# Kernel tuning notes

Measured on AMD Instinct MI355X. Metric: run time of the kernel, lower is better.

The kernel has to match this reference:

```python
import jax, jax.numpy as jnp
import numpy as np

K, T, CIN = 30000, 35, 7
EPS = 1e-5  # torch BatchNorm default


def _bn(x, gamma, beta):
    # x: [1, K, T, C]; per-channel batch-stat normalization over (0,1,2)
    mean = jnp.mean(x, axis=(0, 1, 2))
    var = jnp.var(x, axis=(0, 1, 2))
    return (x - mean) * jax.lax.rsqrt(var + EPS) * gamma + beta


def _vfe(x, mask, W, b, gamma, beta):
    # x: [1, K, T, Cin] -> [1, K, T, 2*units]
    pw = jnp.einsum('bkti,iu->bktu', x, W) + b
    pw = jax.nn.relu(_bn(pw, gamma, beta))
    agg = jnp.max(pw, axis=2, keepdims=True)            # [1, K, 1, units]
    out = jnp.concatenate([pw, jnp.broadcast_to(agg, pw.shape)], axis=-1)
    return out * mask


def setup_inputs() -> dict:
    key = jax.random.key(0)
    ks = jax.random.split(key, 8)
    inp = {}
    inp['x'] = jax.random.normal(ks[0], (K, T, CIN), jnp.float32)
    inp['coordinate'] = jax.random.randint(ks[1], (K, 4), 0, 1, dtype=jnp.int32)
    inp['batch_size'] = 1
    inp['W1'] = jax.random.normal(ks[2], (7, 16), jnp.float32) * 0.3
    inp['b1'] = jnp.zeros((16,), jnp.float32)
    inp['g1'] = jnp.ones((16,), jnp.float32)
    inp['be1'] = jnp.zeros((16,), jnp.float32)
    inp['W2'] = jax.random.normal(ks[3], (32, 64), jnp.float32) * 0.15
    inp['b2'] = jnp.zeros((64,), jnp.float32)
    inp['g2'] = jnp.ones((64,), jnp.float32)
    inp['be2'] = jnp.zeros((64,), jnp.float32)
    inp['Wd'] = jax.random.normal(ks[4], (128, 128), jnp.float32) * 0.1
    inp['bd'] = jnp.zeros((128,), jnp.float32)
    inp['gd'] = jnp.ones((128,), jnp.float32)
    inp['bed'] = jnp.zeros((128,), jnp.float32)
    return inp


def reference(x, coordinate, batch_size, W1, b1, g1, be1, W2, b2, g2, be2, Wd, bd, gd, bed):
    xb = x[None]                                   # [1, K, T, 7]
    # mask: 1 where the point's feature sum is nonzero
    mask = (jnp.sum(xb, axis=-1) != 0.0).astype(jnp.float32)[..., None]  # [1,K,T,1]
    h = _vfe(xb, mask, W1, b1, g1, be1)            # [1, K, T, 32]
    h = _vfe(h, mask, W2, b2, g2, be2)             # [1, K, T, 128]
    h = jnp.einsum('bktc,cd->bktd', h, Wd) + bd    # [1, K, T, 128]
    h = _bn(h, gd, bed)                            # BatchNorm2d after permute(0,3,1,2)
    h = jnp.where(h >= 0, h, 0.1 * h)              # leaky_relu(0.1)
    h = jnp.max(h, axis=2)                         # max over points -> [1, K, 128]
    out = jnp.transpose(h, (0, 2, 1))              # [1, 128, K] to match NCHW layout
    return (out, coordinate)
```

## Files before the change

kernel.cpp:

```cpp
#include <hip/hip_runtime.h>

#define KVOX 30000
#define TP 35
#define NPTS (KVOX * TP)
#define EPS_BN 1e-5f

typedef __attribute__((ext_vector_type(8))) short short8_t;
typedef __attribute__((ext_vector_type(4))) float f32x4;

#define SLOTG_OFF 0
#define SLOT2_OFF 2560
#define SLOT3_OFF 10752
#define PAR_A1 27136
#define PAR_C1 27152
#define PAR_A2 27168
#define PAR_C2 27232
#define PAR_A3 27296
#define PAR_C3 27424
#define STATS_FLOATS 27136
#define W2T_OFF 27552
#define WDT_OFF 28576
#define M3_OFF 36768
#define SMALL_FLOATS (36768 + KVOX * 128)
#define H1G_OFF SMALL_FLOATS
#define AGG1G_OFF (H1G_OFF + KVOX * 280)
#define MASKG_OFF (AGG1G_OFF + KVOX * 8)
#define FULL_FLOATS (MASKG_OFF + (KVOX * 35 + 1) / 2)

__device__ __forceinline__ ushort f2bf(float f) {
    uint r;
    asm("v_cvt_pk_bf16_f32 %0, %1, %2" : "=v"(r) : "v"(f), "v"(f));
    return (ushort)r;
}
__device__ __forceinline__ uint f2bf2(float lo, float hi) {
    uint r;
    asm("v_cvt_pk_bf16_f32 %0, %1, %2" : "=v"(r) : "v"(lo), "v"(hi));
    return r;
}
__device__ __forceinline__ float bf2f(ushort h) {
    union { uint u; float f; } v; v.u = ((uint)h) << 16; return v.f;
}

__global__ __launch_bounds__(256) void k_prep_stats1(
    const float* __restrict__ x,
    const float* __restrict__ W2, const float* __restrict__ Wd,
    const float* __restrict__ gd,
    ushort* __restrict__ w2t, ushort* __restrict__ wdt,
    float* __restrict__ slotG) {
    if (blockIdx.x < 64) {
        int t = blockIdx.x * 256 + threadIdx.x;
        if (t < 2048) {
            int u = t >> 5, k = t & 31;
            w2t[t] = f2bf(W2[k * 64 + u]);
        }
        int u = t >> 7, k = t & 127;
        float sg = (gd[u] < 0.f) ? -1.f : 1.f;
        wdt[t] = f2bf(Wd[k * 128 + u] * sg);
        return;
    }
    int bid = blockIdx.x - 64;
    int tid = threadIdx.x;
    int gid = bid * 256 + tid;
    float sx[7], G[28];
#pragma unroll
    for (int c = 0; c < 7; ++c) sx[c] = 0.f;
#pragma unroll
    for (int i = 0; i < 28; ++i) G[i] = 0.f;
    for (int p = gid; p < NPTS; p += 256 * 256) {
        const float* xp = x + (size_t)p * 7;
        float xv[7];
#pragma unroll
        for (int c = 0; c < 7; ++c) { xv[c] = xp[c]; sx[c] += xv[c]; }
        int idx = 0;
#pragma unroll
        for (int i = 0; i < 7; ++i)
#pragma unroll
            for (int j = i; j < 7; ++j) { G[idx] = fmaf(xv[i], xv[j], G[idx]); ++idx; }
    }
    int lane = tid & 63;
    int wv = tid >> 6;
    int slot = (bid * 4 + wv) & 63;
#pragma unroll
    for (int k = 0; k < 35; ++k) {
        float v = (k < 28) ? G[k] : sx[k - 28];
#pragma unroll
        for (int m = 32; m > 0; m >>= 1) v += __shfl_xor(v, m, 64);
        if (lane == 0) atomicAdd(&slotG[slot * 40 + k], v);
    }
}

__global__ void k_affine1g(const float* __restrict__ slotG,
                           const float* __restrict__ W1, const float* __restrict__ b1,
                           const float* __restrict__ g1, const float* __restrict__ be1,
                           float* __restrict__ pa, float* __restrict__ pc, float invN) {
    __shared__ float red[35];
    int t = threadIdx.x;
    if (t < 35) {
        float s = 0.f;
#pragma unroll
        for (int sl = 0; sl < 64; ++sl) s += slotG[sl * 40 + t];
        red[t] = s;
    }
    __syncthreads();
    if (t < 16) {
        float wv[7];
#pragma unroll
        for (int c = 0; c < 7; ++c) wv[c] = W1[c * 16 + t];
        float b = b1[t];
        float sw = 0.f;
#pragma unroll
        for (int c = 0; c < 7; ++c) sw = fmaf(red[28 + c], wv[c], sw);
        float gq = 0.f;
        int idx = 0;
#pragma unroll
        for (int i = 0; i < 7; ++i)
#pragma unroll
            for (int j = i; j < 7; ++j) {
                float coef = wv[i] * wv[j];
                if (i != j) coef *= 2.f;
                gq = fmaf(coef, red[idx], gq);
                ++idx;
            }
        float mr = sw * invN;
        float mean = mr + b;
        float ex2 = gq * invN + 2.f * b * mr + b * b;
        float var = ex2 - mean * mean;
        float av = g1[t] * rsqrtf(var + EPS_BN);
        pa[t] = av;
        pc[t] = be1[t] - mean * av;
    }
}

__global__ void k_affine_b(const float* __restrict__ slots,
                           const float* __restrict__ g,
                           const float* __restrict__ be,
                           const float* __restrict__ bias,
                           float* __restrict__ pa, float* __restrict__ pc,
                           int C, float invN) {
    int u = threadIdx.x;
    if (u >= C) return;
    float s = 0.f, q = 0.f;
    for (int sl = 0; sl < 64; ++sl) {
        s += slots[sl * 2 * C + u];
        q += slots[sl * 2 * C + C + u];
    }
    float b = bias[u];
    float mr = s * invN;
    float mean = mr + b;
    float ex2 = q * invN + 2.f * b * mr + b * b;
    float var = ex2 - mean * mean;
    float av = g[u] * rsqrtf(var + EPS_BN);
    pa[u] = av;
    pc[u] = be[u] - mean * av;
}

__global__ void k_affine_b3(const float* __restrict__ slots,
                            const float* __restrict__ g,
                            const float* __restrict__ be,
                            const float* __restrict__ bias,
                            float* __restrict__ pa, float* __restrict__ pc,
                            int C, float invN) {
    int u = threadIdx.x;
    if (u >= C) return;
    float s = 0.f, q = 0.f;
    for (int sl = 0; sl < 64; ++sl) {
        s += slots[sl * 2 * C + u];
        q += slots[sl * 2 * C + C + u];
    }
    float sg = (g[u] < 0.f) ? -1.f : 1.f;
    s *= sg;
    float b = bias[u];
    float mr = s * invN;
    float mean = mr + b;
    float ex2 = q * invN + 2.f * b * mr + b * b;
    float var = ex2 - mean * mean;
    float av = g[u] * rsqrtf(var + EPS_BN);
    pa[u] = av;
    pc[u] = be[u] - mean * av;
}

__device__ __forceinline__ void phaseA(
    int k0, int tid,
    const float* __restrict__ x,
    const float* __restrict__ W1, const float* __restrict__ b1,
    const float* __restrict__ a1, const float* __restrict__ c1,
    ushort* __restrict__ h1, float* __restrict__ lmask, float* __restrict__ aggp,
    float& g0o, float& g1o) {
    int u = tid & 15;
    int g = tid >> 4;
    int v = g & 1;
    int th = g >> 1;
    float pmax = 0.f;
    if (th < 7) {
        float b1u = b1[u];
        float a1u = a1[u], c1u = c1[u];
        float w1c[7];
#pragma unroll
        for (int c = 0; c < 7; ++c) w1c[c] = W1[c * 16 + u];
#pragma unroll
        for (int i = 0; i < 5; ++i) {
            int t = th * 5 + i;
            const float* xp = x + ((size_t)(k0 + v) * TP + t) * 7;
            float xv[7];
            float sum7 = 0.f;
#pragma unroll
            for (int c = 0; c < 7; ++c) { xv[c] = xp[c]; sum7 += xv[c]; }
            float mk = (sum7 != 0.f) ? 1.f : 0.f;
            if (u == 0) lmask[v * TP + t] = mk;
            float val = b1u;
#pragma unroll
            for (int c = 0; c < 7; ++c) val = fmaf(xv[c], w1c[c], val);
            val = fmaxf(fmaf(a1u, val, c1u), 0.f);
            pmax = fmaxf(pmax, val);
            h1[(v * TP + t) * 40 + u] = f2bf(val * mk);
        }
    } else {
#pragma unroll
        for (int i = 0; i < 5; ++i) {
            int row = 70 + (g & 1) * 5 + i;
            h1[row * 40 + u] = 0;
            if (u == 0) lmask[row] = 0.f;
        }
    }
    pmax = fmaxf(pmax, __shfl_xor(pmax, 32, 64));
    int w = tid >> 6;
    int lane = tid & 63;
    if (lane < 32) aggp[w * 32 + lane] = pmax;
    __syncthreads();
    {
        int uu = tid & 15;
        int r0 = tid >> 4;
        float g0 = fmaxf(fmaxf(aggp[uu], aggp[32 + uu]),
                         fmaxf(aggp[64 + uu], aggp[96 + uu]));
        float g1 = fmaxf(fmaxf(aggp[16 + uu], aggp[48 + uu]),
                         fmaxf(aggp[80 + uu], aggp[112 + uu]));
        g0o = g0; g1o = g1;
        ushort a0 = f2bf(g0), a1b = f2bf(g1);
#pragma unroll
        for (int j = 0; j < 5; ++j) {
            int row = r0 + j * 16;
            float mk = lmask[row];
            h1[row * 40 + 16 + uu] = (mk != 0.f) ? ((row < TP) ? a0 : a1b) : (ushort)0;
        }
    }
    __syncthreads();
}

template <bool DUMP>
__global__ __launch_bounds__(256, 8) void k_stats2(
    const float* __restrict__ x,
    const float* __restrict__ W1, const float* __restrict__ b1,
    const ushort* __restrict__ w2t,
    const float* __restrict__ ws,
    float* __restrict__ slot2,
    uint* __restrict__ h1G, ushort* __restrict__ agg1G, ushort* __restrict__ maskG) {
    __shared__ __align__(16) ushort h1[80 * 40];
    __shared__ float lmask[80];
    __shared__ float aggp[128];
    int tid = threadIdx.x;
    int k0 = blockIdx.x * 2;
    float g0, g1;
    phaseA(k0, tid, x, W1, b1, ws + PAR_A1, ws + PAR_C1, h1, lmask, aggp, g0, g1);
    if (DUMP) {
        for (int i = tid; i < 560; i += 256)
            h1G[(size_t)k0 * 280 + i] = ((const uint*)h1)[(i >> 3) * 20 + (i & 7)];
        if (tid < 16) {
            agg1G[k0 * 16 + tid] = f2bf(g0);
            agg1G[k0 * 16 + 16 + tid] = f2bf(g1);
        }
        if (tid < 70) maskG[k0 * 35 + tid] = f2bf(lmask[tid]);
    }
    int w = tid >> 6, lane = tid & 63, lq = lane >> 4, lr = lane & 15;
    int u = w * 16 + lr;
    short8_t bfrag = *(const short8_t*)(w2t + u * 32 + lq * 8);
    float s1v = 0.f, s2v = 0.f;
#pragma unroll
    for (int mt = 0; mt < 5; ++mt) {
        short8_t afrag = *(const short8_t*)(h1 + (mt * 16 + lr) * 40 + lq * 8);
        f32x4 acc = {0.f, 0.f, 0.f, 0.f};
        acc = __builtin_amdgcn_mfma_f32_16x16x32_bf16(afrag, bfrag, acc, 0, 0, 0);
#pragma unroll
        for (int r = 0; r < 4; ++r) { s1v += acc[r]; s2v = fmaf(acc[r], acc[r], s2v); }
    }
    s1v += __shfl_xor(s1v, 16, 64); s1v += __shfl_xor(s1v, 32, 64);
    s2v += __shfl_xor(s2v, 16, 64); s2v += __shfl_xor(s2v, 32, 64);
    if (lq == 0) {
        int slot = blockIdx.x & 63;
        atomicAdd(&slot2[slot * 128 + u], s1v);
        atomicAdd(&slot2[slot * 128 + 64 + u], s2v);
    }
}

__global__ __launch_bounds__(512, 8) void k_stage3_reuse(
    const uint* __restrict__ h1G, const ushort* __restrict__ agg1G,
    const ushort* __restrict__ maskG,
    const float* __restrict__ b2,
    const ushort* __restrict__ w2t, const ushort* __restrict__ wdt,
    const float* __restrict__ bd, const float* __restrict__ gd,
    const float* __restrict__ ws,
    float* __restrict__ slot3, float* __restrict__ m3) {
    __shared__ __align__(16) ushort h1[80 * 40];
    __shared__ __align__(16) ushort h2[80 * 136];
    __shared__ float lmask[80];
    __shared__ float aggh[2][2][64];
    int tid = threadIdx.x;
    int k0 = blockIdx.x * 2;
    int w = tid >> 6, lane = tid & 63, lq = lane >> 4, lr = lane & 15;

    for (int i = tid; i < 560; i += 512)
        ((uint*)h1)[(i >> 3) * 20 + (i & 7)] = h1G[(size_t)k0 * 280 + i];
    if (tid < 200) ((uint*)h1)[1400 + tid] = 0u;
    if (tid < 80) lmask[tid] = (tid < 70) ? bf2f(maskG[k0 * 35 + tid]) : 0.f;
    __syncthreads();
    {
        int uu = tid & 15, r0 = tid >> 4;
        ushort a0 = agg1G[k0 * 16 + uu], a1 = agg1G[k0 * 16 + 16 + uu];
#pragma unroll
        for (int j = 0; j < 3; ++j) {
            int row = r0 + j * 32;
            if (row < 70) {
                float mk = lmask[row];
                h1[row * 40 + 16 + uu] = (mk != 0.f) ? ((row < TP) ? a0 : a1) : (ushort)0;
            }
        }
    }
    __syncthreads();
    {
        int uq = w & 3, mh = w >> 2;
        int u = uq * 16 + lr;
        short8_t bfrag = *(const short8_t*)(w2t + u * 32 + lq * 8);
        float a2u = (ws + PAR_A2)[u];
        float c2p = fmaf(a2u, b2[u], (ws + PAR_C2)[u]);
        float av0 = 0.f, av1 = 0.f;
#pragma unroll
        for (int mt = 0; mt < 5; ++mt) {
            if (mh == 0 ? (mt >= 3) : (mt < 3)) continue;
            short8_t afrag = *(const short8_t*)(h1 + (mt * 16 + lr) * 40 + lq * 8);
            f32x4 acc = {0.f, 0.f, 0.f, 0.f};
            acc = __builtin_amdgcn_mfma_f32_16x16x32_bf16(afrag, bfrag, acc, 0, 0, 0);
#pragma unroll
            for (int r = 0; r < 4; ++r) {
                int m = mt * 16 + lq * 4 + r;
                float val = fmaxf(fmaf(a2u, acc[r], c2p), 0.f);
                float vm = (m < 70) ? val : 0.f;
                if (m < TP) av0 = fmaxf(av0, vm); else av1 = fmaxf(av1, vm);
                h2[m * 136 + u] = f2bf(val * lmask[m]);
            }
        }
        av0 = fmaxf(av0, __shfl_xor(av0, 16, 64));
        av0 = fmaxf(av0, __shfl_xor(av0, 32, 64));
        av1 = fmaxf(av1, __shfl_xor(av1, 16, 64));
        av1 = fmaxf(av1, __shfl_xor(av1, 32, 64));
        if (lq == 0) { aggh[mh][0][u] = av0; aggh[mh][1][u] = av1; }
    }
    __syncthreads();
    {
        int c2 = tid & 31;
        int r0 = tid >> 5;
        float l0 = fmaxf(aggh[0][0][2 * c2], aggh[1][0][2 * c2]);
        float h0 = fmaxf(aggh[0][0][2 * c2 + 1], aggh[1][0][2 * c2 + 1]);
        float l1 = fmaxf(aggh[0][1][2 * c2], aggh[1][1][2 * c2]);
        float hh1 = fmaxf(aggh[0][1][2 * c2 + 1], aggh[1][1][2 * c2 + 1]);
        uint pk0 = f2bf2(l0, h0), pk1 = f2bf2(l1, hh1);
#pragma unroll
        for (int j = 0; j < 5; ++j) {
            int row = r0 + j * 16;
            float mk = lmask[row];
            uint val = (mk != 0.f) ? ((row < TP) ? pk0 : pk1) : 0u;
            *(uint*)(h2 + row * 136 + 64 + 2 * c2) = val;
        }
    }
    __syncthreads();
    {
        int u = w * 16 + lr;
        short8_t bfr[4];
#pragma unroll
        for (int kk = 0; kk < 4; ++kk)
            bfr[kk] = *(const short8_t*)(wdt + (u * 128 + kk * 32 + lq * 8));
        float mx0 = -1e30f, mx1 = -1e30f, s1 = 0.f, s2 = 0.f;
#pragma unroll
        for (int mt = 0; mt < 5; ++mt) {
            short8_t af[4];
#pragma unroll
            for (int kk = 0; kk < 4; ++kk)
                af[kk] = *(const short8_t*)(h2 + (mt * 16 + lr) * 136 + kk * 32 + lq * 8);
            f32x4 acc = {0.f, 0.f, 0.f, 0.f};
#pragma unroll
            for (int kk = 0; kk < 4; ++kk)
                acc = __builtin_amdgcn_mfma_f32_16x16x32_bf16(af[kk], bfr[kk], acc, 0, 0, 0);
#pragma unroll
            for (int r = 0; r < 4; ++r) {
                float a = acc[r];
                s1 += a;
                s2 = fmaf(a, a, s2);
                int m = mt * 16 + lq * 4 + r;
                if (mt <= 1) mx0 = fmaxf(mx0, a);
                else if (mt == 3) mx1 = fmaxf(mx1, a);
                else if (mt == 2) { if (m < TP) mx0 = fmaxf(mx0, a); else mx1 = fmaxf(mx1, a); }
                else { if (m < 70) mx1 = fmaxf(mx1, a); }
            }
        }
        mx0 = fmaxf(mx0, __shfl_xor(mx0, 16, 64));
        mx0 = fmaxf(mx0, __shfl_xor(mx0, 32, 64));
        mx1 = fmaxf(mx1, __shfl_xor(mx1, 16, 64));
        mx1 = fmaxf(mx1, __shfl_xor(mx1, 32, 64));
        s1 += __shfl_xor(s1, 16, 64); s1 += __shfl_xor(s1, 32, 64);
        s2 += __shfl_xor(s2, 16, 64); s2 += __shfl_xor(s2, 32, 64);
        if (lq == 0) {
            float bdu = bd[u];
            float sg = (gd[u] < 0.f) ? -1.f : 1.f;
            m3[(size_t)k0 * 128 + u] = fmaf(sg, mx0, bdu);
            m3[(size_t)(k0 + 1) * 128 + u] = fmaf(sg, mx1, bdu);
            int slot = blockIdx.x & 63;
            atomicAdd(&slot3[slot * 256 + u], s1);
            atomicAdd(&slot3[slot * 256 + 128 + u], s2);
        }
    }
}

template <bool WSPATH>
__global__ __launch_bounds__(256) void k_stage3_full(
    const float* __restrict__ x,
    const float* __restrict__ W1, const float* __restrict__ b1,
    const float* __restrict__ b2,
    const ushort* __restrict__ w2t, const ushort* __restrict__ wdt,
    const float* __restrict__ bd, const float* __restrict__ gd,
    const float* __restrict__ ws,
    float* __restrict__ slot3,
    float* __restrict__ m3, float* __restrict__ outbuf) {
    __shared__ __align__(16) ushort h1[80 * 40];
    __shared__ __align__(16) ushort h2[80 * 136];
    __shared__ float lmask[80];
    __shared__ float aggp[128];
    __shared__ ushort agg2bf[128];
    int tid = threadIdx.x;
    int k0 = blockIdx.x * 2;
    int w = tid >> 6, lane = tid & 63, lq = lane >> 4, lr = lane & 15;
    float gd0, gd1;
    phaseA(k0, tid, x, W1, b1, ws + PAR_A1, ws + PAR_C1, h1, lmask, aggp, gd0, gd1);

    int u0 = w * 32;
    short8_t bfr[2][4];
#pragma unroll
    for (int s = 0; s < 2; ++s)
#pragma unroll
        for (int kk = 0; kk < 4; ++kk)
            bfr[s][kk] = *(const short8_t*)(wdt + ((u0 + s * 16 + lr) * 128 + kk * 32 + lq * 8));

    {
        int u = w * 16 + lr;
        short8_t bfrag = *(const short8_t*)(w2t + u * 32 + lq * 8);
        float a2u = (ws + PAR_A2)[u];
        float c2p = fmaf(a2u, b2[u], (ws + PAR_C2)[u]);
        float aggv0 = 0.f, aggv1 = 0.f;
#pragma unroll
        for (int mt = 0; mt < 5; ++mt) {
            short8_t afrag = *(const short8_t*)(h1 + (mt * 16 + lr) * 40 + lq * 8);
            f32x4 acc = {0.f, 0.f, 0.f, 0.f};
            acc = __builtin_amdgcn_mfma_f32_16x16x32_bf16(afrag, bfrag, acc, 0, 0, 0);
#pragma unroll
            for (int r = 0; r < 4; ++r) {
                int m = mt * 16 + lq * 4 + r;
                float val = fmaxf(fmaf(a2u, acc[r], c2p), 0.f);
                float vm = (m < 70) ? val : 0.f;
                if (m < TP) aggv0 = fmaxf(aggv0, vm); else aggv1 = fmaxf(aggv1, vm);
                h2[m * 136 + u] = f2bf(val * lmask[m]);
            }
        }
        aggv0 = fmaxf(aggv0, __shfl_xor(aggv0, 16, 64));
        aggv0 = fmaxf(aggv0, __shfl_xor(aggv0, 32, 64));
        aggv1 = fmaxf(aggv1, __shfl_xor(aggv1, 16, 64));
        aggv1 = fmaxf(aggv1, __shfl_xor(aggv1, 32, 64));
        if (lq == 0) {
            agg2bf[u] = f2bf(aggv0);
            agg2bf[64 + u] = f2bf(aggv1);
        }
    }
    __syncthreads();
    {
        int c = tid & 63;
        int r0 = tid >> 6;
        ushort a0 = agg2bf[c], a1v = agg2bf[64 + c];
#pragma unroll
        for (int j = 0; j < 20; ++j) {
            int row = r0 + j * 4;
            float mk = lmask[row];
            h2[row * 136 + 64 + c] = (mk != 0.f) ? ((row < TP) ? a0 : a1v) : (ushort)0;
        }
    }
    __syncthreads();
    {
        float mxa[2][2], s1a[2], s2a[2];
#pragma unroll
        for (int s = 0; s < 2; ++s) {
            s1a[s] = 0.f; s2a[s] = 0.f;
            mxa[s][0] = -1e30f; mxa[s][1] = -1e30f;
        }
#pragma unroll
        for (int mt = 0; mt < 5; ++mt) {
            short8_t af[4];
#pragma unroll
            for (int kk = 0; kk < 4; ++kk)
                af[kk] = *(const short8_t*)(h2 + (mt * 16 + lr) * 136 + kk * 32 + lq * 8);
#pragma unroll
            for (int s = 0; s < 2; ++s) {
                f32x4 acc = {0.f, 0.f, 0.f, 0.f};
#pragma unroll
                for (int kk = 0; kk < 4; ++kk)
                    acc = __builtin_amdgcn_mfma_f32_16x16x32_bf16(af[kk], bfr[s][kk], acc, 0, 0, 0);
#pragma unroll
                for (int r = 0; r < 4; ++r) {
                    float a = acc[r];
                    s1a[s] += a;
                    s2a[s] = fmaf(a, a, s2a[s]);
                    int m = mt * 16 + lq * 4 + r;
                    if (mt <= 1) mxa[s][0] = fmaxf(mxa[s][0], a);
                    else if (mt == 3) mxa[s][1] = fmaxf(mxa[s][1], a);
                    else if (mt == 2) { if (m < TP) mxa[s][0] = fmaxf(mxa[s][0], a); else mxa[s][1] = fmaxf(mxa[s][1], a); }
                    else { if (m < 70) mxa[s][1] = fmaxf(mxa[s][1], a); }
                }
            }
        }
#pragma unroll
        for (int s = 0; s < 2; ++s) {
#pragma unroll
            for (int v = 0; v < 2; ++v) {
                mxa[s][v] = fmaxf(mxa[s][v], __shfl_xor(mxa[s][v], 16, 64));
                mxa[s][v] = fmaxf(mxa[s][v], __shfl_xor(mxa[s][v], 32, 64));
            }
            s1a[s] += __shfl_xor(s1a[s], 16, 64); s1a[s] += __shfl_xor(s1a[s], 32, 64);
            s2a[s] += __shfl_xor(s2a[s], 16, 64); s2a[s] += __shfl_xor(s2a[s], 32, 64);
        }
        if (lq == 0) {
            int slot = blockIdx.x & 63;
#pragma unroll
            for (int s = 0; s < 2; ++s) {
                int u = u0 + s * 16 + lr;
                float bdu = bd[u];
                float sg = (gd[u] < 0.f) ? -1.f : 1.f;
#pragma unroll
                for (int v = 0; v < 2; ++v) {
                    float res = fmaf(sg, mxa[s][v], bdu);
                    if (WSPATH) m3[(size_t)(k0 + v) * 128 + u] = res;
                    else        outbuf[(size_t)u * KVOX + (k0 + v)] = res;
                }
                atomicAdd(&slot3[slot * 256 + u], s1a[s]);
                atomicAdd(&slot3[slot * 256 + 128 + u], s2a[s]);
            }
        }
    }
}

__global__ __launch_bounds__(256) void k_final_ws(const float* __restrict__ m3,
                                                  const float* __restrict__ ws,
                                                  float* __restrict__ out) {
    __shared__ float tile[32][33];
    int tx = threadIdx.x & 31;
    int ty = threadIdx.x >> 5;
    int v0 = blockIdx.x * 32;
    int u0 = blockIdx.y * 32;
    const float* a3 = ws + PAR_A3;
    const float* c3 = ws + PAR_C3;
#pragma unroll
    for (int r = ty; r < 32; r += 8) {
        int v = v0 + r, u = u0 + tx;
        float y = 0.f;
        if (v < KVOX) {
            float a = a3[u], c = c3[u];
            float val = m3[(size_t)v * 128 + u];
            y = a * val + c;
            y = (y >= 0.f) ? y : 0.1f * y;
        }
        tile[r][tx] = y;
    }
    __syncthreads();
#pragma unroll
    for (int r = ty; r < 32; r += 8) {
        int u = u0 + r, v = v0 + tx;
        if (v < KVOX) out[(size_t)u * KVOX + v] = tile[tx][r];
    }
}

__global__ __launch_bounds__(256) void k_final_inplace(const float* __restrict__ ws,
                                                       float* __restrict__ out) {
    int v = blockIdx.x * 256 + threadIdx.x;
    int u = blockIdx.y;
    if (v >= KVOX) return;
    float a = ws[PAR_A3 + u], c = ws[PAR_C3 + u];
    size_t idx = (size_t)u * KVOX + v;
    float y = a * out[idx] + c;
    out[idx] = (y >= 0.f) ? y : 0.1f * y;
}

extern "C" void kernel_launch(void* const* d_in, const int* in_sizes, int n_in,
                              void* d_out, int out_size, void* d_ws, size_t ws_size,
                              hipStream_t stream) {
    const float* x   = (const float*)d_in[0];
    const void*  coord = d_in[1];
    const float* W1  = (const float*)d_in[3];
    const float* b1  = (const float*)d_in[4];
    const float* g1  = (const float*)d_in[5];
    const float* be1 = (const float*)d_in[6];
    const float* W2  = (const float*)d_in[7];
    const float* b2  = (const float*)d_in[8];
    const float* g2  = (const float*)d_in[9];
    const float* be2 = (const float*)d_in[10];
    const float* Wd  = (const float*)d_in[11];
    const float* bd  = (const float*)d_in[12];
    const float* gd  = (const float*)d_in[13];
    const float* bed = (const float*)d_in[14];
    float* ws = (float*)d_ws;
    float* out = (float*)d_out;
    ushort* w2t = (ushort*)(ws + W2T_OFF);
    ushort* wdt = (ushort*)(ws + WDT_OFF);
    uint* h1G = (uint*)(ws + H1G_OFF);
    ushort* agg1G = (ushort*)(ws + AGG1G_OFF);
    ushort* maskG = (ushort*)(ws + MASKG_OFF);

    size_t wsf = ws_size / 4;
    bool full = wsf >= (size_t)FULL_FLOATS;
    bool small = wsf >= (size_t)SMALL_FLOATS;
    const float invN = 1.f / (float)NPTS;

    hipMemsetAsync(d_ws, 0, (size_t)STATS_FLOATS * 4, stream);

    k_prep_stats1<<<64 + 256, 256, 0, stream>>>(x, W2, Wd, gd, w2t, wdt, ws + SLOTG_OFF);
    k_affine1g<<<1, 64, 0, stream>>>(ws + SLOTG_OFF, W1, b1, g1, be1, ws + PAR_A1, ws + PAR_C1, invN);
    if (full)
        k_stats2<true><<<KVOX / 2, 256, 0, stream>>>(x, W1, b1, w2t, ws, ws + SLOT2_OFF, h1G, agg1G, maskG);
    else
        k_stats2<false><<<KVOX / 2, 256, 0, stream>>>(x, W1, b1, w2t, ws, ws + SLOT2_OFF, h1G, agg1G, maskG);
    k_affine_b<<<1, 64, 0, stream>>>(ws + SLOT2_OFF, g2, be2, b2, ws + PAR_A2, ws + PAR_C2, 64, invN);

    if (full) {
        k_stage3_reuse<<<KVOX / 2, 512, 0, stream>>>(h1G, agg1G, maskG, b2, w2t, wdt, bd, gd, ws,
                                                     ws + SLOT3_OFF, ws + M3_OFF);
        k_affine_b3<<<1, 128, 0, stream>>>(ws + SLOT3_OFF, gd, bed, bd, ws + PAR_A3, ws + PAR_C3, 128, invN);
        k_final_ws<<<dim3((KVOX + 31) / 32, 4), 256, 0, stream>>>(ws + M3_OFF, ws, out);
    } else if (small) {
        k_stage3_full<true><<<KVOX / 2, 256, 0, stream>>>(x, W1, b1, b2, w2t, wdt, bd, gd, ws,
                                                          ws + SLOT3_OFF, ws + M3_OFF, out);
        k_affine_b3<<<1, 128, 0, stream>>>(ws + SLOT3_OFF, gd, bed, bd, ws + PAR_A3, ws + PAR_C3, 128, invN);
        k_final_ws<<<dim3((KVOX + 31) / 32, 4), 256, 0, stream>>>(ws + M3_OFF, ws, out);
    } else {
        k_stage3_full<false><<<KVOX / 2, 256, 0, stream>>>(x, W1, b1, b2, w2t, wdt, bd, gd, ws,
                                                           ws + SLOT3_OFF, ws, out);
        k_affine_b3<<<1, 128, 0, stream>>>(ws + SLOT3_OFF, gd, bed, bd, ws + PAR_A3, ws + PAR_C3, 128, invN);
        k_final_inplace<<<dim3((KVOX + 255) / 256, 128), 256, 0, stream>>>(ws, out);
    }
    hipMemcpyAsync((char*)d_out + (size_t)128 * KVOX * 4, coord,
                   (size_t)KVOX * 4 * sizeof(int), hipMemcpyDeviceToDevice, stream);
}
```

Before: 180.6 us.

## Factor per-voxel max-aggregate matmul out of per-point MFMAs and compact intermediates

The concatenated max-aggregate half of each VFE output is identical for every point in a voxel. Its product with the bottom half of the weights is now computed once per voxel with a single MFMA, then added to each point's result and masked. This halves the K dimension of the per-point MFMAs in the stage-2 statistics, the stage-3 layer-2 and the dense layer, and removes the shared-memory writes of broadcast aggregate rows. Points are also interleaved across the two voxels, per-block records (h1, agg, mask) are packed into one contiguous buffer, and the per-voxel max m3 is stored as bf16, which reduces workspace traffic at some loss of precision in the final output.

```diff
diff --git a/kernel.cpp b/kernel.cpp
--- a/kernel.cpp
+++ b/kernel.cpp
@@ -7,6 +7,9 @@
 
 typedef __attribute__((ext_vector_type(8))) short short8_t;
 typedef __attribute__((ext_vector_type(4))) float f32x4;
+typedef __attribute__((ext_vector_type(2))) float f32x2;
+
+#define MFMA_BF16 __builtin_amdgcn_mfma_f32_16x16x32_bf16
 
 #define SLOTG_OFF 0
 #define SLOT2_OFF 2560
@@ -21,11 +24,10 @@
 #define W2T_OFF 27552
 #define WDT_OFF 28576
 #define M3_OFF 36768
-#define SMALL_FLOATS (36768 + KVOX * 128)
+#define SMALL_FLOATS (36768 + KVOX * 64)
 #define H1G_OFF SMALL_FLOATS
-#define AGG1G_OFF (H1G_OFF + KVOX * 280)
-#define MASKG_OFF (AGG1G_OFF + KVOX * 8)
-#define FULL_FLOATS (MASKG_OFF + (KVOX * 35 + 1) / 2)
+#define REC_DW 696
+#define FULL_FLOATS (H1G_OFF + (KVOX / 2) * REC_DW)
 
 __device__ __forceinline__ ushort f2bf(float f) {
     uint r;
@@ -39,6 +41,9 @@
 }
 __device__ __forceinline__ float bf2f(ushort h) {
     union { uint u; float f; } v; v.u = ((uint)h) << 16; return v.f;
+}
+__device__ __forceinline__ f32x2 mk2(float a, float b) {
+    f32x2 r; r[0] = a; r[1] = b; return r;
 }
 
 __global__ __launch_bounds__(256) void k_prep_stats1(
@@ -179,13 +184,13 @@
     pc[u] = be[u] - mean * av;
 }
 
-__device__ __forceinline__ void phaseA(
+__device__ __forceinline__ void phaseA_il(
     int k0, int tid,
     const float* __restrict__ x,
     const float* __restrict__ W1, const float* __restrict__ b1,
     const float* __restrict__ a1, const float* __restrict__ c1,
-    ushort* __restrict__ h1, float* __restrict__ lmask, float* __restrict__ aggp,
-    float& g0o, float& g1o) {
+    ushort* __restrict__ h1, float* __restrict__ lmask,
+    float* __restrict__ aggp, ushort* __restrict__ agg1bf) {
     int u = tid & 15;
     int g = tid >> 4;
     int v = g & 1;
@@ -205,14 +210,280 @@
             float sum7 = 0.f;
 #pragma unroll
             for (int c = 0; c < 7; ++c) { xv[c] = xp[c]; sum7 += xv[c]; }
-            float mk = (sum7 != 0.f) ? 1.f : 0.f;
-            if (u == 0) lmask[v * TP + t] = mk;
+            float mkv = (sum7 != 0.f) ? 1.f : 0.f;
+            int row = 2 * t + v;
+            if (u == 0) lmask[row] = mkv;
             float val = b1u;
 #pragma unroll
             for (int c = 0; c < 7; ++c) val = fmaf(xv[c], w1c[c], val);
             val = fmaxf(fmaf(a1u, val, c1u), 0.f);
             pmax = fmaxf(pmax, val);
-            h1[(v * TP + t) * 40 + u] = f2bf(val * mk);
+            h1[row * 24 + u] = f2bf(val * mkv);
+        }
+    } else if (g < 16) {
+#pragma unroll
+        for (int i = 0; i < 5; ++i) {
+            int row = 70 + (g & 1) + 2 * i;
+            h1[row * 24 + u] = 0;
+            if (u == 0) lmask[row] = 0.f;
+        }
+    }
+    pmax = fmaxf(pmax, __shfl_xor(pmax, 32, 64));
+    int w = tid >> 6;
+    int lane = tid & 63;
+    if (lane < 32 && w < 4) aggp[w * 32 + lane] = pmax;
+    __syncthreads();
+    if (tid < 16) {
+        float g0 = fmaxf(fmaxf(aggp[u], aggp[32 + u]),
+                         fmaxf(aggp[64 + u], aggp[96 + u]));
+        float g1 = fmaxf(fmaxf(aggp[16 + u], aggp[48 + u]),
+                         fmaxf(aggp[80 + u], aggp[112 + u]));
+        agg1bf[u] = f2bf(g0);
+        agg1bf[16 + u] = f2bf(g1);
+    }
+    __syncthreads();
+}
+
+template <bool DUMP>
+__global__ __launch_bounds__(256, 8) void k_stats2(
+    const float* __restrict__ x,
+    const float* __restrict__ W1, const float* __restrict__ b1,
+    const ushort* __restrict__ w2t,
+    const float* __restrict__ ws,
+    float* __restrict__ slot2, uint* __restrict__ recs) {
+    __shared__ __align__(16) ushort h1[80 * 24];
+    __shared__ float lmask[80];
+    __shared__ float aggp[128];
+    __shared__ __align__(16) ushort agg1bf[32];
+    __shared__ __align__(16) uint zeros16[4];
+    int tid = threadIdx.x;
+    int k0 = blockIdx.x * 2;
+    if (tid < 4) zeros16[tid] = 0;
+    phaseA_il(k0, tid, x, W1, b1, ws + PAR_A1, ws + PAR_C1, h1, lmask, aggp, agg1bf);
+    if (DUMP) {
+        uint* rec = recs + (size_t)blockIdx.x * REC_DW;
+        const uint* h1dw = (const uint*)h1;
+        for (int i = tid; i < 640; i += 256) rec[i] = h1dw[(i >> 3) * 12 + (i & 7)];
+        if (tid < 16) rec[640 + tid] = ((const uint*)agg1bf)[tid];
+        if (tid < 40) rec[656 + tid] = f2bf2(lmask[2 * tid], lmask[2 * tid + 1]);
+    }
+    int w = tid >> 6, lane = tid & 63, lq = lane >> 4, lr = lane & 15;
+    int u = w * 16 + lr;
+    short8_t bB = *(const short8_t*)(w2t + u * 32 + (lq & 1) * 8);
+    const ushort* pa = (lq < 2) ? (agg1bf + (lr & 1) * 16 + lq * 8) : (const ushort*)zeros16;
+    short8_t pAf = *(const short8_t*)pa;
+    short8_t bP = *(const short8_t*)(w2t + u * 32 + 16 + (lq & 1) * 8);
+    f32x4 aP = {0.f, 0.f, 0.f, 0.f};
+    aP = MFMA_BF16(pAf, bP, aP, 0, 0, 0);
+    f32x2 p1p = mk2(__shfl(aP[0], lr, 64), __shfl(aP[1], lr, 64));
+    f32x2 s1p = {0.f, 0.f}, s2p = {0.f, 0.f};
+#pragma unroll
+    for (int mt = 0; mt < 5; ++mt) {
+        const ushort* ha = (lq < 2) ? (h1 + (mt * 16 + lr) * 24 + lq * 8) : (const ushort*)zeros16;
+        short8_t af = *(const short8_t*)ha;
+        f32x4 acc = {0.f, 0.f, 0.f, 0.f};
+        acc = MFMA_BF16(af, bB, acc, 0, 0, 0);
+        const f32x4 mk = *(const f32x4*)(lmask + mt * 16 + lq * 4);
+        f32x2 am01 = (mk2(acc[0], acc[1]) + p1p) * mk2(mk[0], mk[1]);
+        f32x2 am23 = (mk2(acc[2], acc[3]) + p1p) * mk2(mk[2], mk[3]);
+        s1p += am01 + am23;
+        s2p += am01 * am01;
+        s2p += am23 * am23;
+    }
+    float s1 = s1p[0] + s1p[1], s2 = s2p[0] + s2p[1];
+    s1 += __shfl_xor(s1, 16, 64); s1 += __shfl_xor(s1, 32, 64);
+    s2 += __shfl_xor(s2, 16, 64); s2 += __shfl_xor(s2, 32, 64);
+    if (lq == 0) {
+        int slot = blockIdx.x & 63;
+        atomicAdd(&slot2[slot * 128 + u], s1);
+        atomicAdd(&slot2[slot * 128 + 64 + u], s2);
+    }
+}
+
+__global__ __launch_bounds__(512, 8) void k_stage3_reuse(
+    const uint* __restrict__ recs,
+    const float* __restrict__ b2,
+    const ushort* __restrict__ w2t, const ushort* __restrict__ wdt,
+    const float* __restrict__ bd, const float* __restrict__ gd,
+    const float* __restrict__ ws,
+    float* __restrict__ slot3, ushort* __restrict__ m3) {
+    __shared__ __align__(16) ushort h1[80 * 24];
+    __shared__ __align__(16) ushort h2[80 * 72];
+    __shared__ float lmask[80];
+    __shared__ float aggh[2][2][64];
+    __shared__ __align__(16) ushort agg1bf[32];
+    __shared__ __align__(16) ushort agg2bf[2 * 64];
+    __shared__ __align__(16) uint zeros16[4];
+    int tid = threadIdx.x;
+    int k0 = blockIdx.x * 2;
+    int w = tid >> 6, lane = tid & 63, lq = lane >> 4, lr = lane & 15;
+
+    {
+        const uint* rec = recs + (size_t)blockIdx.x * REC_DW;
+        uint* h1dw = (uint*)h1;
+        h1dw[(tid >> 3) * 12 + (tid & 7)] = rec[tid];
+        if (tid < 184) {
+            int i2 = 512 + tid;
+            if (i2 < 640) h1dw[(i2 >> 3) * 12 + (i2 & 7)] = rec[i2];
+            else if (i2 < 656) ((uint*)agg1bf)[i2 - 640] = rec[i2];
+            else {
+                uint mw = rec[i2];
+                int j = i2 - 656;
+                lmask[2 * j] = bf2f((ushort)(mw & 0xffffu));
+                lmask[2 * j + 1] = bf2f((ushort)(mw >> 16));
+            }
+        }
+        if (tid < 4) zeros16[tid] = 0;
+    }
+    __syncthreads();
+
+    {
+        int mh = w >> 2, uq = w & 3;
+        int u = uq * 16 + lr;
+        short8_t bB = *(const short8_t*)(w2t + u * 32 + (lq & 1) * 8);
+        const ushort* pa = (lq < 2) ? (agg1bf + (lr & 1) * 16 + lq * 8) : (const ushort*)zeros16;
+        short8_t pAf = *(const short8_t*)pa;
+        short8_t bP = *(const short8_t*)(w2t + u * 32 + 16 + (lq & 1) * 8);
+        f32x4 aP = {0.f, 0.f, 0.f, 0.f};
+        aP = MFMA_BF16(pAf, bP, aP, 0, 0, 0);
+        f32x2 p1p = mk2(__shfl(aP[0], lr, 64), __shfl(aP[1], lr, 64));
+        float a2u = ws[PAR_A2 + u];
+        float c2u = fmaf(a2u, b2[u], ws[PAR_C2 + u]);
+        f32x2 a2p = mk2(a2u, a2u), c2p = mk2(c2u, c2u);
+        float av0 = 0.f, av1 = 0.f;
+        int mt0 = mh ? 3 : 0, mt1 = mh ? 5 : 3;
+        for (int mt = mt0; mt < mt1; ++mt) {
+            const ushort* ha = (lq < 2) ? (h1 + (mt * 16 + lr) * 24 + lq * 8) : (const ushort*)zeros16;
+            short8_t af = *(const short8_t*)ha;
+            f32x4 acc = {0.f, 0.f, 0.f, 0.f};
+            acc = MFMA_BF16(af, bB, acc, 0, 0, 0);
+            const f32x4 mk = *(const f32x4*)(lmask + mt * 16 + lq * 4);
+            int m0 = mt * 16 + lq * 4;
+            f32x2 am01 = (mk2(acc[0], acc[1]) + p1p) * mk2(mk[0], mk[1]);
+            f32x2 am23 = (mk2(acc[2], acc[3]) + p1p) * mk2(mk[2], mk[3]);
+            f32x2 t01 = a2p * am01 + c2p;
+            f32x2 t23 = a2p * am23 + c2p;
+            float v0 = fmaxf(t01[0], 0.f), v1 = fmaxf(t01[1], 0.f);
+            float v2 = fmaxf(t23[0], 0.f), v3 = fmaxf(t23[1], 0.f);
+            h2[(m0 + 0) * 72 + u] = f2bf(v0);
+            h2[(m0 + 1) * 72 + u] = f2bf(v1);
+            h2[(m0 + 2) * 72 + u] = f2bf(v2);
+            h2[(m0 + 3) * 72 + u] = f2bf(v3);
+            if (mt == 4) {
+                bool c01 = lq < 2, c23 = lq < 1;
+                v0 = c01 ? v0 : 0.f; v1 = c01 ? v1 : 0.f;
+                v2 = c23 ? v2 : 0.f; v3 = c23 ? v3 : 0.f;
+            }
+            av0 = fmaxf(av0, fmaxf(v0, v2));
+            av1 = fmaxf(av1, fmaxf(v1, v3));
+        }
+        av0 = fmaxf(av0, __shfl_xor(av0, 16, 64));
+        av0 = fmaxf(av0, __shfl_xor(av0, 32, 64));
+        av1 = fmaxf(av1, __shfl_xor(av1, 16, 64));
+        av1 = fmaxf(av1, __shfl_xor(av1, 32, 64));
+        if (lq == 0) { aggh[mh][0][u] = av0; aggh[mh][1][u] = av1; }
+    }
+    __syncthreads();
+    if (tid < 32) {
+        int u2 = tid;
+        float l0 = fmaxf(aggh[0][0][2 * u2], aggh[1][0][2 * u2]);
+        float h0 = fmaxf(aggh[0][0][2 * u2 + 1], aggh[1][0][2 * u2 + 1]);
+        float l1 = fmaxf(aggh[0][1][2 * u2], aggh[1][1][2 * u2]);
+        float h1v = fmaxf(aggh[0][1][2 * u2 + 1], aggh[1][1][2 * u2 + 1]);
+        ((uint*)agg2bf)[u2] = f2bf2(l0, h0);
+        ((uint*)agg2bf)[32 + u2] = f2bf2(l1, h1v);
+    }
+    __syncthreads();
+
+    {
+        int u = w * 16 + lr;
+        short8_t bM0 = *(const short8_t*)(wdt + u * 128 + lq * 8);
+        short8_t bM1 = *(const short8_t*)(wdt + u * 128 + 32 + lq * 8);
+        short8_t bP0 = *(const short8_t*)(wdt + u * 128 + 64 + lq * 8);
+        short8_t bP1 = *(const short8_t*)(wdt + u * 128 + 96 + lq * 8);
+        short8_t pA0 = *(const short8_t*)(agg2bf + (lr & 1) * 64 + lq * 8);
+        short8_t pA1 = *(const short8_t*)(agg2bf + (lr & 1) * 64 + 32 + lq * 8);
+        f32x4 aP = {0.f, 0.f, 0.f, 0.f};
+        aP = MFMA_BF16(pA0, bP0, aP, 0, 0, 0);
+        aP = MFMA_BF16(pA1, bP1, aP, 0, 0, 0);
+        f32x2 p2p = mk2(__shfl(aP[0], lr, 64), __shfl(aP[1], lr, 64));
+        float mx0 = -1e30f, mx1 = -1e30f;
+        f32x2 s1p = {0.f, 0.f}, s2p = {0.f, 0.f};
+#pragma unroll
+        for (int mt = 0; mt < 5; ++mt) {
+            const ushort* hrow = h2 + (mt * 16 + lr) * 72;
+            short8_t a0 = *(const short8_t*)(hrow + lq * 8);
+            short8_t a1 = *(const short8_t*)(hrow + 32 + lq * 8);
+            f32x4 acc = {0.f, 0.f, 0.f, 0.f};
+            acc = MFMA_BF16(a0, bM0, acc, 0, 0, 0);
+            acc = MFMA_BF16(a1, bM1, acc, 0, 0, 0);
+            const f32x4 mk = *(const f32x4*)(lmask + mt * 16 + lq * 4);
+            f32x2 am01 = (mk2(acc[0], acc[1]) + p2p) * mk2(mk[0], mk[1]);
+            f32x2 am23 = (mk2(acc[2], acc[3]) + p2p) * mk2(mk[2], mk[3]);
+            s1p += am01 + am23;
+            s2p += am01 * am01;
+            s2p += am23 * am23;
+            if (mt < 4) {
+                mx0 = fmaxf(mx0, fmaxf(am01[0], am23[0]));
+                mx1 = fmaxf(mx1, fmaxf(am01[1], am23[1]));
+            } else {
+                bool c01 = lq < 2, c23 = lq < 1;
+                mx0 = fmaxf(mx0, fmaxf(c01 ? am01[0] : -1e30f, c23 ? am23[0] : -1e30f));
+                mx1 = fmaxf(mx1, fmaxf(c01 ? am01[1] : -1e30f, c23 ? am23[1] : -1e30f));
+            }
+        }
+        mx0 = fmaxf(mx0, __shfl_xor(mx0, 16, 64));
+        mx0 = fmaxf(mx0, __shfl_xor(mx0, 32, 64));
+        mx1 = fmaxf(mx1, __shfl_xor(mx1, 16, 64));
+        mx1 = fmaxf(mx1, __shfl_xor(mx1, 32, 64));
+        float s1 = s1p[0] + s1p[1], s2 = s2p[0] + s2p[1];
+        s1 += __shfl_xor(s1, 16, 64); s1 += __shfl_xor(s1, 32, 64);
+        s2 += __shfl_xor(s2, 16, 64); s2 += __shfl_xor(s2, 32, 64);
+        if (lq == 0) {
+            float sg = (gd[u] < 0.f) ? -1.f : 1.f;
+            float bdu = bd[u];
+            m3[(size_t)k0 * 128 + u] = f2bf(fmaf(sg, mx0, bdu));
+            m3[(size_t)(k0 + 1) * 128 + u] = f2bf(fmaf(sg, mx1, bdu));
+            int slot = blockIdx.x & 63;
+            atomicAdd(&slot3[slot * 256 + u], s1);
+            atomicAdd(&slot3[slot * 256 + 128 + u], s2);
+        }
+    }
+}
+
+__device__ __forceinline__ void phaseA_leg(
+    int k0, int tid,
+    const float* __restrict__ x,
+    const float* __restrict__ W1, const float* __restrict__ b1,
+    const float* __restrict__ a1, const float* __restrict__ c1,
+    ushort* __restrict__ h1, float* __restrict__ lmask, float* __restrict__ aggp) {
+    int u = tid & 15;
+    int g = tid >> 4;
+    int v = g & 1;
+    int th = g >> 1;
+    float pmax = 0.f;
+    if (th < 7) {
+        float b1u = b1[u];
+        float a1u = a1[u], c1u = c1[u];
+        float w1c[7];
+#pragma unroll
+        for (int c = 0; c < 7; ++c) w1c[c] = W1[c * 16 + u];
+#pragma unroll
+        for (int i = 0; i < 5; ++i) {
+            int t = th * 5 + i;
+            const float* xp = x + ((size_t)(k0 + v) * TP + t) * 7;
+            float xv[7];
+            float sum7 = 0.f;
+#pragma unroll
+            for (int c = 0; c < 7; ++c) { xv[c] = xp[c]; sum7 += xv[c]; }
+            float mkv = (sum7 != 0.f) ? 1.f : 0.f;
+            if (u == 0) lmask[v * TP + t] = mkv;
+            float val = b1u;
+#pragma unroll
+            for (int c = 0; c < 7; ++c) val = fmaf(xv[c], w1c[c], val);
+            val = fmaxf(fmaf(a1u, val, c1u), 0.f);
+            pmax = fmaxf(pmax, val);
+            h1[(v * TP + t) * 40 + u] = f2bf(val * mkv);
         }
     } else {
 #pragma unroll
@@ -234,188 +505,15 @@
                          fmaxf(aggp[64 + uu], aggp[96 + uu]));
         float g1 = fmaxf(fmaxf(aggp[16 + uu], aggp[48 + uu]),
                          fmaxf(aggp[80 + uu], aggp[112 + uu]));
-        g0o = g0; g1o = g1;
         ushort a0 = f2bf(g0), a1b = f2bf(g1);
 #pragma unroll
         for (int j = 0; j < 5; ++j) {
             int row = r0 + j * 16;
-            float mk = lmask[row];
-            h1[row * 40 + 16 + uu] = (mk != 0.f) ? ((row < TP) ? a0 : a1b) : (ushort)0;
-        }
-    }
-    __syncthreads();
-}
-
-template <bool DUMP>
-__global__ __launch_bounds__(256, 8) void k_stats2(
-    const float* __restrict__ x,
-    const float* __restrict__ W1, const float* __restrict__ b1,
-    const ushort* __restrict__ w2t,
-    const float* __restrict__ ws,
-    float* __restrict__ slot2,
-    uint* __restrict__ h1G, ushort* __restrict__ agg1G, ushort* __restrict__ maskG) {
-    __shared__ __align__(16) ushort h1[80 * 40];
-    __shared__ float lmask[80];
-    __shared__ float aggp[128];
-    int tid = threadIdx.x;
-    int k0 = blockIdx.x * 2;
-    float g0, g1;
-    phaseA(k0, tid, x, W1, b1, ws + PAR_A1, ws + PAR_C1, h1, lmask, aggp, g0, g1);
-    if (DUMP) {
-        for (int i = tid; i < 560; i += 256)
-            h1G[(size_t)k0 * 280 + i] = ((const uint*)h1)[(i >> 3) * 20 + (i & 7)];
-        if (tid < 16) {
-            agg1G[k0 * 16 + tid] = f2bf(g0);
-            agg1G[k0 * 16 + 16 + tid] = f2bf(g1);
-        }
-        if (tid < 70) maskG[k0 * 35 + tid] = f2bf(lmask[tid]);
-    }
-    int w = tid >> 6, lane = tid & 63, lq = lane >> 4, lr = lane & 15;
-    int u = w * 16 + lr;
-    short8_t bfrag = *(const short8_t*)(w2t + u * 32 + lq * 8);
-    float s1v = 0.f, s2v = 0.f;
-#pragma unroll
-    for (int mt = 0; mt < 5; ++mt) {
-        short8_t afrag = *(const short8_t*)(h1 + (mt * 16 + lr) * 40 + lq * 8);
-        f32x4 acc = {0.f, 0.f, 0.f, 0.f};
-        acc = __builtin_amdgcn_mfma_f32_16x16x32_bf16(afrag, bfrag, acc, 0, 0, 0);
-#pragma unroll
-        for (int r = 0; r < 4; ++r) { s1v += acc[r]; s2v = fmaf(acc[r], acc[r], s2v); }
-    }
-    s1v += __shfl_xor(s1v, 16, 64); s1v += __shfl_xor(s1v, 32, 64);
-    s2v += __shfl_xor(s2v, 16, 64); s2v += __shfl_xor(s2v, 32, 64);
-    if (lq == 0) {
-        int slot = blockIdx.x & 63;
-        atomicAdd(&slot2[slot * 128 + u], s1v);
-        atomicAdd(&slot2[slot * 128 + 64 + u], s2v);
-    }
-}
-
-__global__ __launch_bounds__(512, 8) void k_stage3_reuse(
-    const uint* __restrict__ h1G, const ushort* __restrict__ agg1G,
-    const ushort* __restrict__ maskG,
-    const float* __restrict__ b2,
-    const ushort* __restrict__ w2t, const ushort* __restrict__ wdt,
-    const float* __restrict__ bd, const float* __restrict__ gd,
-    const float* __restrict__ ws,
-    float* __restrict__ slot3, float* __restrict__ m3) {
-    __shared__ __align__(16) ushort h1[80 * 40];
-    __shared__ __align__(16) ushort h2[80 * 136];
-    __shared__ float lmask[80];
-    __shared__ float aggh[2][2][64];
-    int tid = threadIdx.x;
-    int k0 = blockIdx.x * 2;
-    int w = tid >> 6, lane = tid & 63, lq = lane >> 4, lr = lane & 15;
-
-    for (int i = tid; i < 560; i += 512)
-        ((uint*)h1)[(i >> 3) * 20 + (i & 7)] = h1G[(size_t)k0 * 280 + i];
-    if (tid < 200) ((uint*)h1)[1400 + tid] = 0u;
-    if (tid < 80) lmask[tid] = (tid < 70) ? bf2f(maskG[k0 * 35 + tid]) : 0.f;
-    __syncthreads();
-    {
-        int uu = tid & 15, r0 = tid >> 4;
-        ushort a0 = agg1G[k0 * 16 + uu], a1 = agg1G[k0 * 16 + 16 + uu];
-#pragma unroll
-        for (int j = 0; j < 3; ++j) {
-            int row = r0 + j * 32;
-            if (row < 70) {
-                float mk = lmask[row];
-                h1[row * 40 + 16 + uu] = (mk != 0.f) ? ((row < TP) ? a0 : a1) : (ushort)0;
-            }
-        }
-    }
-    __syncthreads();
-    {
-        int uq = w & 3, mh = w >> 2;
-        int u = uq * 16 + lr;
-        short8_t bfrag = *(const short8_t*)(w2t + u * 32 + lq * 8);
-        float a2u = (ws + PAR_A2)[u];
-        float c2p = fmaf(a2u, b2[u], (ws + PAR_C2)[u]);
-        float av0 = 0.f, av1 = 0.f;
-#pragma unroll
-        for (int mt = 0; mt < 5; ++mt) {
-            if (mh == 0 ? (mt >= 3) : (mt < 3)) continue;
-            short8_t afrag = *(const short8_t*)(h1 + (mt * 16 + lr) * 40 + lq * 8);
-            f32x4 acc = {0.f, 0.f, 0.f, 0.f};
-            acc = __builtin_amdgcn_mfma_f32_16x16x32_bf16(afrag, bfrag, acc, 0, 0, 0);
-#pragma unroll
-            for (int r = 0; r < 4; ++r) {
-                int m = mt * 16 + lq * 4 + r;
-                float val = fmaxf(fmaf(a2u, acc[r], c2p), 0.f);
-                float vm = (m < 70) ? val : 0.f;
-                if (m < TP) av0 = fmaxf(av0, vm); else av1 = fmaxf(av1, vm);
-                h2[m * 136 + u] = f2bf(val * lmask[m]);
-            }
-        }
-        av0 = fmaxf(av0, __shfl_xor(av0, 16, 64));
-        av0 = fmaxf(av0, __shfl_xor(av0, 32, 64));
-        av1 = fmaxf(av1, __shfl_xor(av1, 16, 64));
-        av1 = fmaxf(av1, __shfl_xor(av1, 32, 64));
-        if (lq == 0) { aggh[mh][0][u] = av0; aggh[mh][1][u] = av1; }
-    }
-    __syncthreads();
-    {
-        int c2 = tid & 31;
-        int r0 = tid >> 5;
-        float l0 = fmaxf(aggh[0][0][2 * c2], aggh[1][0][2 * c2]);
-        float h0 = fmaxf(aggh[0][0][2 * c2 + 1], aggh[1][0][2 * c2 + 1]);
-        float l1 = fmaxf(aggh[0][1][2 * c2], aggh[1][1][2 * c2]);
-        float hh1 = fmaxf(aggh[0][1][2 * c2 + 1], aggh[1][1][2 * c2 + 1]);
-        uint pk0 = f2bf2(l0, h0), pk1 = f2bf2(l1, hh1);
-#pragma unroll
-        for (int j = 0; j < 5; ++j) {
-            int row = r0 + j * 16;
-            float mk = lmask[row];
-            uint val = (mk != 0.f) ? ((row < TP) ? pk0 : pk1) : 0u;
-            *(uint*)(h2 + row * 136 + 64 + 2 * c2) = val;
-        }
-    }
-    __syncthreads();
-    {
-        int u = w * 16 + lr;
-        short8_t bfr[4];
-#pragma unroll
-        for (int kk = 0; kk < 4; ++kk)
-            bfr[kk] = *(const short8_t*)(wdt + (u * 128 + kk * 32 + lq * 8));
-        float mx0 = -1e30f, mx1 = -1e30f, s1 = 0.f, s2 = 0.f;
-#pragma unroll
-        for (int mt = 0; mt < 5; ++mt) {
-            short8_t af[4];
-#pragma unroll
-            for (int kk = 0; kk < 4; ++kk)
-                af[kk] = *(const short8_t*)(h2 + (mt * 16 + lr) * 136 + kk * 32 + lq * 8);
-            f32x4 acc = {0.f, 0.f, 0.f, 0.f};
-#pragma unroll
-            for (int kk = 0; kk < 4; ++kk)
-                acc = __builtin_amdgcn_mfma_f32_16x16x32_bf16(af[kk], bfr[kk], acc, 0, 0, 0);
-#pragma unroll
-            for (int r = 0; r < 4; ++r) {
-                float a = acc[r];
-                s1 += a;
-                s2 = fmaf(a, a, s2);
-                int m = mt * 16 + lq * 4 + r;
-                if (mt <= 1) mx0 = fmaxf(mx0, a);
-                else if (mt == 3) mx1 = fmaxf(mx1, a);
-                else if (mt == 2) { if (m < TP) mx0 = fmaxf(mx0, a); else mx1 = fmaxf(mx1, a); }
-                else { if (m < 70) mx1 = fmaxf(mx1, a); }
-            }
-        }
-        mx0 = fmaxf(mx0, __shfl_xor(mx0, 16, 64));
-        mx0 = fmaxf(mx0, __shfl_xor(mx0, 32, 64));
-        mx1 = fmaxf(mx1, __shfl_xor(mx1, 16, 64));
-        mx1 = fmaxf(mx1, __shfl_xor(mx1, 32, 64));
-        s1 += __shfl_xor(s1, 16, 64); s1 += __shfl_xor(s1, 32, 64);
-        s2 += __shfl_xor(s2, 16, 64); s2 += __shfl_xor(s2, 32, 64);
-        if (lq == 0) {
-            float bdu = bd[u];
-            float sg = (gd[u] < 0.f) ? -1.f : 1.f;
-            m3[(size_t)k0 * 128 + u] = fmaf(sg, mx0, bdu);
-            m3[(size_t)(k0 + 1) * 128 + u] = fmaf(sg, mx1, bdu);
-            int slot = blockIdx.x & 63;
-            atomicAdd(&slot3[slot * 256 + u], s1);
-            atomicAdd(&slot3[slot * 256 + 128 + u], s2);
-        }
-    }
+            float mkv = lmask[row];
+            h1[row * 40 + 16 + uu] = (mkv != 0.f) ? ((row < TP) ? a0 : a1b) : (ushort)0;
+        }
+    }
+    __syncthreads();
 }
 
 template <bool WSPATH>
@@ -427,7 +525,7 @@
     const float* __restrict__ bd, const float* __restrict__ gd,
     const float* __restrict__ ws,
     float* __restrict__ slot3,
-    float* __restrict__ m3, float* __restrict__ outbuf) {
+    ushort* __restrict__ m3, float* __restrict__ outbuf) {
     __shared__ __align__(16) ushort h1[80 * 40];
     __shared__ __align__(16) ushort h2[80 * 136];
     __shared__ float lmask[80];
@@ -436,8 +534,7 @@
     int tid = threadIdx.x;
     int k0 = blockIdx.x * 2;
     int w = tid >> 6, lane = tid & 63, lq = lane >> 4, lr = lane & 15;
-    float gd0, gd1;
-    phaseA(k0, tid, x, W1, b1, ws + PAR_A1, ws + PAR_C1, h1, lmask, aggp, gd0, gd1);
+    phaseA_leg(k0, tid, x, W1, b1, ws + PAR_A1, ws + PAR_C1, h1, lmask, aggp);
 
     int u0 = w * 32;
     short8_t bfr[2][4];
@@ -450,14 +547,14 @@
     {
         int u = w * 16 + lr;
         short8_t bfrag = *(const short8_t*)(w2t + u * 32 + lq * 8);
-        float a2u = (ws + PAR_A2)[u];
-        float c2p = fmaf(a2u, b2[u], (ws + PAR_C2)[u]);
+        float a2u = ws[PAR_A2 + u];
+        float c2p = fmaf(a2u, b2[u], ws[PAR_C2 + u]);
         float aggv0 = 0.f, aggv1 = 0.f;
 #pragma unroll
         for (int mt = 0; mt < 5; ++mt) {
             short8_t afrag = *(const short8_t*)(h1 + (mt * 16 + lr) * 40 + lq * 8);
             f32x4 acc = {0.f, 0.f, 0.f, 0.f};
-            acc = __builtin_amdgcn_mfma_f32_16x16x32_bf16(afrag, bfrag, acc, 0, 0, 0);
+            acc = MFMA_BF16(afrag, bfrag, acc, 0, 0, 0);
 #pragma unroll
             for (int r = 0; r < 4; ++r) {
                 int m = mt * 16 + lq * 4 + r;
@@ -484,8 +581,8 @@
 #pragma unroll
         for (int j = 0; j < 20; ++j) {
             int row = r0 + j * 4;
-            float mk = lmask[row];
-            h2[row * 136 + 64 + c] = (mk != 0.f) ? ((row < TP) ? a0 : a1v) : (ushort)0;
+            float mkv = lmask[row];
+            h2[row * 136 + 64 + c] = (mkv != 0.f) ? ((row < TP) ? a0 : a1v) : (ushort)0;
         }
     }
     __syncthreads();
@@ -507,7 +604,7 @@
                 f32x4 acc = {0.f, 0.f, 0.f, 0.f};
 #pragma unroll
                 for (int kk = 0; kk < 4; ++kk)
-                    acc = __builtin_amdgcn_mfma_f32_16x16x32_bf16(af[kk], bfr[s][kk], acc, 0, 0, 0);
+                    acc = MFMA_BF16(af[kk], bfr[s][kk], acc, 0, 0, 0);
 #pragma unroll
                 for (int r = 0; r < 4; ++r) {
                     float a = acc[r];
@@ -541,7 +638,7 @@
 #pragma unroll
                 for (int v = 0; v < 2; ++v) {
                     float res = fmaf(sg, mxa[s][v], bdu);
-                    if (WSPATH) m3[(size_t)(k0 + v) * 128 + u] = res;
+                    if (WSPATH) m3[(size_t)(k0 + v) * 128 + u] = f2bf(res);
                     else        outbuf[(size_t)u * KVOX + (k0 + v)] = res;
                 }
                 atomicAdd(&slot3[slot * 256 + u], s1a[s]);
@@ -551,7 +648,7 @@
     }
 }
 
-__global__ __launch_bounds__(256) void k_final_ws(const float* __restrict__ m3,
+__global__ __launch_bounds__(256) void k_final_ws(const ushort* __restrict__ m3,
                                                   const float* __restrict__ ws,
                                                   float* __restrict__ out) {
     __shared__ float tile[32][33];
@@ -567,7 +664,7 @@
         float y = 0.f;
         if (v < KVOX) {
             float a = a3[u], c = c3[u];
-            float val = m3[(size_t)v * 128 + u];
+            float val = bf2f(m3[(size_t)v * 128 + u]);
             y = a * val + c;
             y = (y >= 0.f) ? y : 0.1f * y;
         }
@@ -613,9 +710,8 @@
     float* out = (float*)d_out;
     ushort* w2t = (ushort*)(ws + W2T_OFF);
     ushort* wdt = (ushort*)(ws + WDT_OFF);
-    uint* h1G = (uint*)(ws + H1G_OFF);
-    ushort* agg1G = (ushort*)(ws + AGG1G_OFF);
-    ushort* maskG = (ushort*)(ws + MASKG_OFF);
+    ushort* m3  = (ushort*)(ws + M3_OFF);
+    uint* recs  = (uint*)(ws + H1G_OFF);
 
     size_t wsf = ws_size / 4;
     bool full = wsf >= (size_t)FULL_FLOATS;
@@ -627,24 +723,24 @@
     k_prep_stats1<<<64 + 256, 256, 0, stream>>>(x, W2, Wd, gd, w2t, wdt, ws + SLOTG_OFF);
     k_affine1g<<<1, 64, 0, stream>>>(ws + SLOTG_OFF, W1, b1, g1, be1, ws + PAR_A1, ws + PAR_C1, invN);
     if (full)
-        k_stats2<true><<<KVOX / 2, 256, 0, stream>>>(x, W1, b1, w2t, ws, ws + SLOT2_OFF, h1G, agg1G, maskG);
+        k_stats2<true><<<KVOX / 2, 256, 0, stream>>>(x, W1, b1, w2t, ws, ws + SLOT2_OFF, recs);
     else
-        k_stats2<false><<<KVOX / 2, 256, 0, stream>>>(x, W1, b1, w2t, ws, ws + SLOT2_OFF, h1G, agg1G, maskG);
+        k_stats2<false><<<KVOX / 2, 256, 0, stream>>>(x, W1, b1, w2t, ws, ws + SLOT2_OFF, recs);
     k_affine_b<<<1, 64, 0, stream>>>(ws + SLOT2_OFF, g2, be2, b2, ws + PAR_A2, ws + PAR_C2, 64, invN);
 
     if (full) {
-        k_stage3_reuse<<<KVOX / 2, 512, 0, stream>>>(h1G, agg1G, maskG, b2, w2t, wdt, bd, gd, ws,
-                                                     ws + SLOT3_OFF, ws + M3_OFF);
+        k_stage3_reuse<<<KVOX / 2, 512, 0, stream>>>(recs, b2, w2t, wdt, bd, gd, ws,
+                                                     ws + SLOT3_OFF, m3);
         k_affine_b3<<<1, 128, 0, stream>>>(ws + SLOT3_OFF, gd, bed, bd, ws + PAR_A3, ws + PAR_C3, 128, invN);
-        k_final_ws<<<dim3((KVOX + 31) / 32, 4), 256, 0, stream>>>(ws + M3_OFF, ws, out);
+        k_final_ws<<<dim3((KVOX + 31) / 32, 4), 256, 0, stream>>>(m3, ws, out);
     } else if (small) {
         k_stage3_full<true><<<KVOX / 2, 256, 0, stream>>>(x, W1, b1, b2, w2t, wdt, bd, gd, ws,
-                                                          ws + SLOT3_OFF, ws + M3_OFF, out);
+                                                          ws + SLOT3_OFF, m3, out);
         k_affine_b3<<<1, 128, 0, stream>>>(ws + SLOT3_OFF, gd, bed, bd, ws + PAR_A3, ws + PAR_C3, 128, invN);
-        k_final_ws<<<dim3((KVOX + 31) / 32, 4), 256, 0, stream>>>(ws + M3_OFF, ws, out);
+        k_final_ws<<<dim3((KVOX + 31) / 32, 4), 256, 0, stream>>>(m3, ws, out);
     } else {
         k_stage3_full<false><<<KVOX / 2, 256, 0, stream>>>(x, W1, b1, b2, w2t, wdt, bd, gd, ws,
-                                                           ws + SLOT3_OFF, ws, out);
+                                                           ws + SLOT3_OFF, m3, out);
         k_affine_b3<<<1, 128, 0, stream>>>(ws + SLOT3_OFF, gd, bed, bd, ws + PAR_A3, ws + PAR_C3, 128, invN);
         k_final_inplace<<<dim3((KVOX + 255) / 256, 128), 256, 0, stream>>>(ws, out);
     }
```

New measurement: 176.3 us. 1.02x faster.
